# Performance work log

Measured on AMD Instinct MI355X. Metric: run time of the kernel, lower is better.

## Reference

```python
import math
import jax, jax.numpy as jnp
import numpy as np

B, T, C = 2, 2048, 1024
N_HEAD = 16
HEAD_DIM = C // N_HEAD


def setup_inputs() -> dict:
    key = jax.random.key(0)
    k1, k2, k3 = jax.random.split(key, 3)
    std = 0.02
    return {
        "x": jax.random.normal(k1, (B, T, C), dtype=jnp.float32),
        "W_qkv": jax.random.normal(k2, (3 * C, C), dtype=jnp.float32) * std,
        "b_qkv": jnp.zeros((3 * C,), dtype=jnp.float32),
        "W_proj": jax.random.normal(k3, (C, C), dtype=jnp.float32) * std,
        "b_proj": jnp.zeros((C,), dtype=jnp.float32),
    }


def reference(x, W_qkv, b_qkv, W_proj, b_proj):
    Bs, Ts, Cs = x.shape
    # qkv projection, split as [3][n_head][head_dim] along last dim (matches torch view order)
    qkv = (x @ W_qkv.T + b_qkv).reshape(Bs, Ts, 3, N_HEAD, HEAD_DIM)
    qkv = qkv.transpose(0, 3, 2, 1, 4)  # (B, H, 3, T, hd)
    q, k, v = qkv[:, :, 0], qkv[:, :, 1], qkv[:, :, 2]  # each (B, H, T, hd)
    scale = 1.0 / math.sqrt(HEAD_DIM)
    att = jnp.einsum('bhtd,bhsd->bhts', q, k) * scale  # (B, H, T, T)
    causal = jnp.tril(jnp.ones((Ts, Ts), dtype=bool))
    att = jnp.where(causal, att, -jnp.inf)
    att = jax.nn.softmax(att, axis=-1)
    y = jnp.einsum('bhts,bhsd->bhtd', att, v)  # (B, H, T, hd)
    y = y.transpose(0, 2, 1, 3).reshape(Bs, Ts, Cs)
    return y @ W_proj.T + b_proj
```

## Files before the change

kernel.cpp:

```cpp
#include <hip/hip_runtime.h>
#include <cstdint>

#define BDIM  2
#define TSEQ  2048
#define CDIM  1024
#define NHEAD 16
#define HDIM  64
#define C3    3072

typedef __attribute__((ext_vector_type(8))) short short8_t;
typedef __attribute__((ext_vector_type(4))) short short4_t;
typedef __attribute__((ext_vector_type(4))) float f32x4;

static __device__ __forceinline__ unsigned short f2bf(float f) {
  union { float f; unsigned u; } v; v.f = f;
  unsigned r = v.u + 0x7FFFu + ((v.u >> 16) & 1u);
  return (unsigned short)(r >> 16);
}
static __device__ __forceinline__ unsigned cvtpk_bf16(float lo, float hi) {
  unsigned r;
  asm("v_cvt_pk_bf16_f32 %0, %1, %2" : "=v"(r) : "v"(lo), "v"(hi));
  return r;
}
static __device__ __forceinline__ void g2lds16(const unsigned short* g,
                                               unsigned short* l) {
  __builtin_amdgcn_global_load_lds(
      (const __attribute__((address_space(1))) void*)g,
      (__attribute__((address_space(3))) void*)l, 16, 0, 0);
}

__device__ __forceinline__ int kk_idx(int row, int chunk) {
  return row * 64 + (((chunk ^ (row & 7)) & 7) << 3);
}
__device__ __forceinline__ int vv_idx(int d, int chunk) {
  return d * 64 + (((chunk ^ (d & 7) ^ ((d >> 3) & 7)) & 7) << 3);
}

__global__ __launch_bounds__(256) void f32_to_bf16_3(
    const float* __restrict__ x, const float* __restrict__ wq,
    const float* __restrict__ wp, unsigned short* __restrict__ outb,
    int n1, int n2, int n3)
{
  const int i = blockIdx.x * 256 + threadIdx.x;
  const float* src; unsigned short* dst; int j;
  if (i < n1)            { src = x;  dst = outb;                        j = i; }
  else if (i < n1 + n2)  { src = wq; dst = outb + (size_t)n1 * 4;       j = i - n1; }
  else if (i < n1+n2+n3) { src = wp; dst = outb + (size_t)(n1+n2) * 4;  j = i - n1 - n2; }
  else return;
  const float4 v = ((const float4*)src)[j];
  const unsigned lo = (unsigned)f2bf(v.x) | ((unsigned)f2bf(v.y) << 16);
  const unsigned hi = (unsigned)f2bf(v.z) | ((unsigned)f2bf(v.w) << 16);
  ((uint2*)dst)[j] = make_uint2(lo, hi);
}

template <int FJ, bool OUT_BF16>
__global__ __launch_bounds__(256, 2) void gemm_bt_mfma(
    const unsigned short* __restrict__ A, const unsigned short* __restrict__ B,
    const float* __restrict__ bias, void* __restrict__ Cv,
    int M, int N, int K)
{
  __shared__ unsigned short As[128 * 64];
  __shared__ unsigned short Bs[FJ * 32 * 64];

  const int tid  = threadIdx.x;
  const int lane = tid & 63;
  const int wv   = tid >> 6;
  const int wr   = wv >> 1, wc = wv & 1;
  const int l15  = lane & 15, g = lane >> 4;
  const int bn = blockIdx.x, bm = blockIdx.y;

  const int srow = tid >> 3;
  const int chg  = (tid & 7) ^ (srow & 7);
  const unsigned short* Ab = A + (size_t)(bm * 128 + srow) * K + chg * 8;
  const unsigned short* Bb = B + (size_t)(bn * (FJ * 32) + srow) * K + chg * 8;

  f32x4 acc[4][FJ];
#pragma unroll
  for (int i = 0; i < 4; ++i)
#pragma unroll
    for (int j = 0; j < FJ; ++j) acc[i][j] = (f32x4){0.f, 0.f, 0.f, 0.f};

  for (int k0 = 0; k0 < K; k0 += 64) {
    __syncthreads();
#pragma unroll
    for (int c = 0; c < 4; ++c)
      g2lds16(Ab + (size_t)(c * 32) * K + k0, &As[c * 2048 + wv * 512]);
#pragma unroll
    for (int c = 0; c < FJ; ++c)
      g2lds16(Bb + (size_t)(c * 32) * K + k0, &Bs[c * 2048 + wv * 512]);
    __syncthreads();

#pragma unroll
    for (int kk = 0; kk < 2; ++kk) {
      short8_t af[4], bf[FJ];
#pragma unroll
      for (int i = 0; i < 4; ++i)
        af[i] = *(const short8_t*)&As[kk_idx(wr * 64 + i * 16 + l15, kk * 4 + g)];
#pragma unroll
      for (int j = 0; j < FJ; ++j)
        bf[j] = *(const short8_t*)&Bs[kk_idx(wc * (FJ * 16) + j * 16 + l15, kk * 4 + g)];
#pragma unroll
      for (int i = 0; i < 4; ++i)
#pragma unroll
        for (int j = 0; j < FJ; ++j)
          acc[i][j] = __builtin_amdgcn_mfma_f32_16x16x32_bf16(af[i], bf[j], acc[i][j], 0, 0, 0);
    }
  }

#pragma unroll
  for (int j = 0; j < FJ; ++j) {
    const int col = bn * (FJ * 32) + wc * (FJ * 16) + j * 16 + l15;
    const float bj = bias[col];
#pragma unroll
    for (int i = 0; i < 4; ++i) {
#pragma unroll
      for (int r = 0; r < 4; ++r) {
        const int row = bm * 128 + wr * 64 + i * 16 + g * 4 + r;
        const float v = acc[i][j][r] + bj;
        if (OUT_BF16) ((unsigned short*)Cv)[(size_t)row * N + col] = f2bf(v);
        else          ((float*)Cv)[(size_t)row * N + col] = v;
      }
    }
  }
}

__global__ __launch_bounds__(512, 2) void attn_mfma(
    const unsigned short* __restrict__ qkv, unsigned short* __restrict__ yb)
{
  __shared__ unsigned short SM[21504];
  unsigned short* Ks = SM;
  unsigned short* Vt = SM + 8192;
  unsigned short* Ps = SM + 16384;

  const int tid  = threadIdx.x;
  const int lane = tid & 63;
  const int wv   = tid >> 6;
  const int qs   = wv & 3;
  const int kvh  = wv >> 2;
  const int l15  = lane & 15, g = lane >> 4;

  const int nfl = blockIdx.x;
  const int x   = (nfl >> 3) & 15;
  const int grp = (nfl & 7) | ((nfl >> 7) << 3);
  const int h = grp & 15, b = grp >> 4;

  const unsigned short* kbase = qkv + (size_t)(b * TSEQ) * C3 + CDIM + h * HDIM;
  const unsigned short* vbase = kbase + CDIM;
  unsigned short* Pw = &Ps[wv * 640];

  const float SC2 = 0.18033688011112042f;
  const float THR = 11.5415603f;

  const int skv = tid >> 3, sc = tid & 7;
  const int kwo = kk_idx(skv, sc);
  const int vs = tid >> 4, dh = (tid >> 3) & 1, va = tid & 7;
  int vwo[4];
#pragma unroll
  for (int j = 0; j < 4; ++j)
    vwo[j] = vv_idx(va * 8 + dh * 4 + j, vs >> 2) + ((2 * vs) & 7);

  int tg = 0;

  for (int ph = 0; ph < 2; ++ph) {
    const int qt   = ph ? (31 - x) : x;
    const int wq0  = qt * 64 + qs * 16;
    const int q_hi = wq0 + 15;
    const int qg   = wq0 + l15;
    const int ntiles = qt + 1;

    short8_t qf[2];
#pragma unroll
    for (int kk = 0; kk < 2; ++kk)
      qf[kk] = *(const short8_t*)(qkv +
          (size_t)(b * TSEQ + wq0 + l15) * C3 + h * HDIM + kk * 32 + g * 8);

    f32x4 O[4];
#pragma unroll
    for (int n = 0; n < 4; ++n) O[n] = (f32x4){0.f, 0.f, 0.f, 0.f};
    float Mr = 0.0f, Lr = 0.f;

    const unsigned short* kptr  = kbase + (size_t)skv * C3 + sc * 8;
    const unsigned short* vptr0 = vbase + (size_t)(2 * vs) * C3 + va * 8 + dh * 4;
    const unsigned short* vptr1 = vptr0 + C3;
    short8_t pk  = *(const short8_t*)(kptr);
    short4_t pv0 = *(const short4_t*)(vptr0);
    short4_t pv1 = *(const short4_t*)(vptr1);

    for (int t = 0; t < ntiles; ++t) {
      const int par = tg & 1;
      unsigned short* Kc = &Ks[par * 4096];
      unsigned short* Vc = &Vt[par * 4096];
      tg++;
      *(short8_t*)&Kc[kwo] = pk;
      {
        const unsigned short* e0 = (const unsigned short*)&pv0;
        const unsigned short* e1 = (const unsigned short*)&pv1;
#pragma unroll
        for (int j = 0; j < 4; ++j)
          *(unsigned*)&Vc[vwo[j]] = (unsigned)e0[j] | ((unsigned)e1[j] << 16);
      }
      __syncthreads();
      if (t + 1 < ntiles) {
        kptr  += (size_t)64 * C3;
        vptr0 += (size_t)64 * C3;
        vptr1 += (size_t)64 * C3;
        pk  = *(const short8_t*)(kptr);
        pv0 = *(const short4_t*)(vptr0);
        pv1 = *(const short4_t*)(vptr1);
      }
      const int kvw0 = t * 64 + kvh * 32;
      if (kvw0 > q_hi) continue;
      const int nl = (q_hi - kvw0) >> 4;
      const int nlim = (nl > 1) ? 1 : nl;

      f32x4 s[2];
#pragma unroll
      for (int n = 0; n < 2; ++n) s[n] = (f32x4){0.f, 0.f, 0.f, 0.f};
      __builtin_amdgcn_s_setprio(1);
#pragma unroll
      for (int n = 0; n < 2; ++n) {
        if (n <= nlim) {
#pragma unroll
          for (int kk = 0; kk < 2; ++kk) {
            const short8_t kf =
                *(const short8_t*)&Kc[kk_idx(kvh * 32 + n * 16 + l15, kk * 4 + g)];
            s[n] = __builtin_amdgcn_mfma_f32_16x16x32_bf16(kf, qf[kk], s[n], 0, 0, 0);
          }
        }
      }
      __builtin_amdgcn_s_setprio(0);

      float mt = -3.0e38f;
#pragma unroll
      for (int n = 0; n < 2; ++n) {
        if (n <= nlim) {
          const int kvb = kvw0 + n * 16 + g * 4;
          const bool needmask = (kvw0 + n * 16 + 15 > wq0);
#pragma unroll
          for (int r = 0; r < 4; ++r) {
            float v = s[n][r] * SC2;
            if (needmask && (kvb + r > qg)) v = -3.0e38f;
            s[n][r] = v;
            mt = fmaxf(mt, v);
          }
        }
      }

      float rs = 0.f;
#pragma unroll
      for (int n = 0; n < 2; ++n) {
        if (n <= nlim) {
#pragma unroll
          for (int r = 0; r < 4; ++r) {
            const float p = __builtin_amdgcn_exp2f(s[n][r] - Mr);
            s[n][r] = p;
            rs += p;
          }
        }
      }
#pragma unroll
      for (int n = 0; n < 2; ++n) {
        const unsigned u0 = cvtpk_bf16(s[n][0], s[n][1]);
        const unsigned u1 = cvtpk_bf16(s[n][2], s[n][3]);
        *(uint2*)&Pw[l15 * 40 + n * 16 + (g << 2)] = make_uint2(u0, u1);
      }
      mt = fmaxf(mt, __shfl_xor(mt, 16));
      mt = fmaxf(mt, __shfl_xor(mt, 32));
      if (__any(mt > Mr + THR)) {
        const float nm = fmaxf(Mr, mt);
        const float al = __builtin_amdgcn_exp2f(Mr - nm);
        Lr *= al;
        rs *= al;
        float alq[4];
#pragma unroll
        for (int r = 0; r < 4; ++r) alq[r] = __shfl(al, (g << 2) + r);
#pragma unroll
        for (int n = 0; n < 4; ++n)
#pragma unroll
          for (int r = 0; r < 4; ++r) O[n][r] *= alq[r];
        Mr = nm;
#pragma unroll
        for (int n = 0; n < 2; ++n) {
          if (n <= nlim) {
#pragma unroll
            for (int r = 0; r < 4; ++r) s[n][r] *= al;
          }
          const unsigned u0 = cvtpk_bf16(s[n][0], s[n][1]);
          const unsigned u1 = cvtpk_bf16(s[n][2], s[n][3]);
          *(uint2*)&Pw[l15 * 40 + n * 16 + (g << 2)] = make_uint2(u0, u1);
        }
      }

      const short8_t pf = *(const short8_t*)&Pw[l15 * 40 + g * 8];
      __builtin_amdgcn_s_setprio(1);
#pragma unroll
      for (int n = 0; n < 4; ++n) {
        const short8_t vf = *(const short8_t*)&Vc[vv_idx(n * 16 + l15, kvh * 4 + g)];
        O[n] = __builtin_amdgcn_mfma_f32_16x16x32_bf16(pf, vf, O[n], 0, 0, 0);
      }
      __builtin_amdgcn_s_setprio(0);

      rs += __shfl_xor(rs, 16);
      rs += __shfl_xor(rs, 32);
      Lr += rs;
    }

    __syncthreads();
    {
      float* Cb = (float*)SM;
      const int slot = (qs * 64 + lane) * 18;
      if (kvh == 1) {
#pragma unroll
        for (int n = 0; n < 4; ++n)
#pragma unroll
          for (int r = 0; r < 4; ++r) Cb[slot + n * 4 + r] = O[n][r];
        Cb[slot + 16] = Mr;
        Cb[slot + 17] = Lr;
      }
    }
    __syncthreads();
    if (kvh == 0) {
      const float* Cb = (const float*)SM;
      const int slot = (qs * 64 + lane) * 18;
      const float m2 = Cb[slot + 16], l2 = Cb[slot + 17];
      const float m  = fmaxf(Mr, m2);
      const float a1 = __builtin_amdgcn_exp2f(Mr - m);
      const float a2 = __builtin_amdgcn_exp2f(m2 - m);
      const float inv = 1.0f / (Lr * a1 + l2 * a2);
      const float fa = a1 * inv, fb = a2 * inv;
      float faq[4], fbq[4];
#pragma unroll
      for (int r = 0; r < 4; ++r) {
        faq[r] = __shfl(fa, (g << 2) + r);
        fbq[r] = __shfl(fb, (g << 2) + r);
      }
#pragma unroll
      for (int n = 0; n < 4; ++n)
#pragma unroll
        for (int r = 0; r < 4; ++r) {
          const float o2 = Cb[slot + n * 4 + r];
          const size_t row = (size_t)(b * TSEQ + wq0 + (g << 2) + r);
          yb[row * CDIM + h * HDIM + n * 16 + l15] =
              f2bf(O[n][r] * faq[r] + o2 * fbq[r]);
        }
    }
    __syncthreads();
  }
}

extern "C" void kernel_launch(void* const* d_in, const int* in_sizes, int n_in,
                              void* d_out, int out_size, void* d_ws, size_t ws_size,
                              hipStream_t stream)
{
  const float* x     = (const float*)d_in[0];
  const float* Wqkv  = (const float*)d_in[1];
  const float* bqkv  = (const float*)d_in[2];
  const float* Wproj = (const float*)d_in[3];
  const float* bproj = (const float*)d_in[4];
  float* out = (float*)d_out;

  const int M = BDIM * TSEQ;
  unsigned short* qkv = (unsigned short*)d_ws;
  unsigned short* yb  = qkv + (size_t)M * C3;
  unsigned short* xb  = yb  + (size_t)M * CDIM;
  unsigned short* wqb = xb  + (size_t)M * CDIM;
  unsigned short* wpb = wqb + (size_t)C3 * CDIM;

  const int n1 = M * CDIM / 4, n2 = C3 * CDIM / 4, n3 = CDIM * CDIM / 4;
  f32_to_bf16_3<<<(n1 + n2 + n3 + 255) / 256, 256, 0, stream>>>(
      x, Wqkv, Wproj, xb, n1, n2, n3);

  gemm_bt_mfma<4, true><<<dim3(C3 / 128, M / 128), 256, 0, stream>>>(
      xb, wqb, bqkv, (void*)qkv, M, C3, CDIM);

  attn_mfma<<<dim3(512, 1, 1), 512, 0, stream>>>(qkv, yb);

  gemm_bt_mfma<2, false><<<dim3(CDIM / 64, M / 128), 256, 0, stream>>>(
      yb, wpb, bproj, (void*)out, M, CDIM, CDIM);
}
```

Baseline: 107.5 us.

## Add unmasked fast path in attention, lighter barriers, and smaller proj GEMM tiles

Attention adds a fast path for fully unmasked KV tiles that skips per-element masking and fuses scale into the exp argument. It defers the cross-lane max reduction into the rare rescale branch and replaces __syncthreads with an lgkmcnt wait plus barrier. The combine buffer moves to a separate LDS region so the trailing barrier can go. The GEMM is templated on the M tile, and the output projection now uses 64x64 tiles with higher occupancy hints for more blocks.

```diff
diff --git a/kernel.cpp b/kernel.cpp
--- a/kernel.cpp
+++ b/kernel.cpp
@@ -27,6 +27,9 @@
   __builtin_amdgcn_global_load_lds(
       (const __attribute__((address_space(1))) void*)g,
       (__attribute__((address_space(3))) void*)l, 16, 0, 0);
+}
+static __device__ __forceinline__ void bar_lds() {
+  asm volatile("s_waitcnt lgkmcnt(0)\n\ts_barrier" ::: "memory");
 }
 
 __device__ __forceinline__ int kk_idx(int row, int chunk) {
@@ -53,13 +56,13 @@
   ((uint2*)dst)[j] = make_uint2(lo, hi);
 }
 
-template <int FJ, bool OUT_BF16>
-__global__ __launch_bounds__(256, 2) void gemm_bt_mfma(
+template <int FI, int FJ, bool OUT_BF16>
+__global__ __launch_bounds__(256, (FI == 4) ? 3 : 4) void gemm_bt_mfma(
     const unsigned short* __restrict__ A, const unsigned short* __restrict__ B,
     const float* __restrict__ bias, void* __restrict__ Cv,
     int M, int N, int K)
 {
-  __shared__ unsigned short As[128 * 64];
+  __shared__ unsigned short As[FI * 32 * 64];
   __shared__ unsigned short Bs[FJ * 32 * 64];
 
   const int tid  = threadIdx.x;
@@ -71,19 +74,19 @@
 
   const int srow = tid >> 3;
   const int chg  = (tid & 7) ^ (srow & 7);
-  const unsigned short* Ab = A + (size_t)(bm * 128 + srow) * K + chg * 8;
+  const unsigned short* Ab = A + (size_t)(bm * (FI * 32) + srow) * K + chg * 8;
   const unsigned short* Bb = B + (size_t)(bn * (FJ * 32) + srow) * K + chg * 8;
 
-  f32x4 acc[4][FJ];
-#pragma unroll
-  for (int i = 0; i < 4; ++i)
+  f32x4 acc[FI][FJ];
+#pragma unroll
+  for (int i = 0; i < FI; ++i)
 #pragma unroll
     for (int j = 0; j < FJ; ++j) acc[i][j] = (f32x4){0.f, 0.f, 0.f, 0.f};
 
   for (int k0 = 0; k0 < K; k0 += 64) {
     __syncthreads();
 #pragma unroll
-    for (int c = 0; c < 4; ++c)
+    for (int c = 0; c < FI; ++c)
       g2lds16(Ab + (size_t)(c * 32) * K + k0, &As[c * 2048 + wv * 512]);
 #pragma unroll
     for (int c = 0; c < FJ; ++c)
@@ -92,15 +95,15 @@
 
 #pragma unroll
     for (int kk = 0; kk < 2; ++kk) {
-      short8_t af[4], bf[FJ];
-#pragma unroll
-      for (int i = 0; i < 4; ++i)
-        af[i] = *(const short8_t*)&As[kk_idx(wr * 64 + i * 16 + l15, kk * 4 + g)];
+      short8_t af[FI], bf[FJ];
+#pragma unroll
+      for (int i = 0; i < FI; ++i)
+        af[i] = *(const short8_t*)&As[kk_idx(wr * (FI * 16) + i * 16 + l15, kk * 4 + g)];
 #pragma unroll
       for (int j = 0; j < FJ; ++j)
         bf[j] = *(const short8_t*)&Bs[kk_idx(wc * (FJ * 16) + j * 16 + l15, kk * 4 + g)];
 #pragma unroll
-      for (int i = 0; i < 4; ++i)
+      for (int i = 0; i < FI; ++i)
 #pragma unroll
         for (int j = 0; j < FJ; ++j)
           acc[i][j] = __builtin_amdgcn_mfma_f32_16x16x32_bf16(af[i], bf[j], acc[i][j], 0, 0, 0);
@@ -112,10 +115,10 @@
     const int col = bn * (FJ * 32) + wc * (FJ * 16) + j * 16 + l15;
     const float bj = bias[col];
 #pragma unroll
-    for (int i = 0; i < 4; ++i) {
+    for (int i = 0; i < FI; ++i) {
 #pragma unroll
       for (int r = 0; r < 4; ++r) {
-        const int row = bm * 128 + wr * 64 + i * 16 + g * 4 + r;
+        const int row = bm * (FI * 32) + wr * (FI * 16) + i * 16 + g * 4 + r;
         const float v = acc[i][j][r] + bj;
         if (OUT_BF16) ((unsigned short*)Cv)[(size_t)row * N + col] = f2bf(v);
         else          ((float*)Cv)[(size_t)row * N + col] = v;
@@ -127,7 +130,7 @@
 __global__ __launch_bounds__(512, 2) void attn_mfma(
     const unsigned short* __restrict__ qkv, unsigned short* __restrict__ yb)
 {
-  __shared__ unsigned short SM[21504];
+  __shared__ unsigned short SM[25600];
   unsigned short* Ks = SM;
   unsigned short* Vt = SM + 8192;
   unsigned short* Ps = SM + 16384;
@@ -147,6 +150,7 @@
   const unsigned short* kbase = qkv + (size_t)(b * TSEQ) * C3 + CDIM + h * HDIM;
   const unsigned short* vbase = kbase + CDIM;
   unsigned short* Pw = &Ps[wv * 640];
+  float* Cb = (float*)Ps;
 
   const float SC2 = 0.18033688011112042f;
   const float THR = 11.5415603f;
@@ -199,7 +203,7 @@
         for (int j = 0; j < 4; ++j)
           *(unsigned*)&Vc[vwo[j]] = (unsigned)e0[j] | ((unsigned)e1[j] << 16);
       }
-      __syncthreads();
+      bar_lds();
       if (t + 1 < ntiles) {
         kptr  += (size_t)64 * C3;
         vptr0 += (size_t)64 * C3;
@@ -210,8 +214,9 @@
       }
       const int kvw0 = t * 64 + kvh * 32;
       if (kvw0 > q_hi) continue;
+      const bool fullt = (kvw0 + 31 <= wq0);
       const int nl = (q_hi - kvw0) >> 4;
-      const int nlim = (nl > 1) ? 1 : nl;
+      const int nlim = fullt ? 1 : ((nl > 1) ? 1 : nl);
 
       f32x4 s[2];
 #pragma unroll
@@ -230,43 +235,58 @@
       }
       __builtin_amdgcn_s_setprio(0);
 
-      float mt = -3.0e38f;
-#pragma unroll
-      for (int n = 0; n < 2; ++n) {
-        if (n <= nlim) {
-          const int kvb = kvw0 + n * 16 + g * 4;
-          const bool needmask = (kvw0 + n * 16 + 15 > wq0);
+      float mt = -3.0e38f, rs = 0.f;
+      if (fullt) {
+#pragma unroll
+        for (int n = 0; n < 2; ++n)
+#pragma unroll
+          for (int r = 0; r < 4; ++r) mt = fmaxf(mt, s[n][r]);
+        mt *= SC2;
+#pragma unroll
+        for (int n = 0; n < 2; ++n)
 #pragma unroll
           for (int r = 0; r < 4; ++r) {
-            float v = s[n][r] * SC2;
-            if (needmask && (kvb + r > qg)) v = -3.0e38f;
-            s[n][r] = v;
-            mt = fmaxf(mt, v);
-          }
-        }
-      }
-
-      float rs = 0.f;
-#pragma unroll
-      for (int n = 0; n < 2; ++n) {
-        if (n <= nlim) {
-#pragma unroll
-          for (int r = 0; r < 4; ++r) {
-            const float p = __builtin_amdgcn_exp2f(s[n][r] - Mr);
+            const float p = __builtin_amdgcn_exp2f(fmaf(s[n][r], SC2, -Mr));
             s[n][r] = p;
             rs += p;
           }
-        }
-      }
+      } else {
+#pragma unroll
+        for (int n = 0; n < 2; ++n) {
+          if (n <= nlim) {
+            const int kvb = kvw0 + n * 16 + g * 4;
+            const bool needmask = (kvw0 + n * 16 + 15 > wq0);
+#pragma unroll
+            for (int r = 0; r < 4; ++r) {
+              float v = s[n][r] * SC2;
+              if (needmask && (kvb + r > qg)) v = -3.0e38f;
+              s[n][r] = v;
+              mt = fmaxf(mt, v);
+            }
+          }
+        }
+#pragma unroll
+        for (int n = 0; n < 2; ++n) {
+          if (n <= nlim) {
+#pragma unroll
+            for (int r = 0; r < 4; ++r) {
+              const float p = __builtin_amdgcn_exp2f(s[n][r] - Mr);
+              s[n][r] = p;
+              rs += p;
+            }
+          }
+        }
+      }
+
 #pragma unroll
       for (int n = 0; n < 2; ++n) {
         const unsigned u0 = cvtpk_bf16(s[n][0], s[n][1]);
         const unsigned u1 = cvtpk_bf16(s[n][2], s[n][3]);
         *(uint2*)&Pw[l15 * 40 + n * 16 + (g << 2)] = make_uint2(u0, u1);
       }
-      mt = fmaxf(mt, __shfl_xor(mt, 16));
-      mt = fmaxf(mt, __shfl_xor(mt, 32));
       if (__any(mt > Mr + THR)) {
+        mt = fmaxf(mt, __shfl_xor(mt, 16));
+        mt = fmaxf(mt, __shfl_xor(mt, 32));
         const float nm = fmaxf(Mr, mt);
         const float al = __builtin_amdgcn_exp2f(Mr - nm);
         Lr *= al;
@@ -281,10 +301,8 @@
         Mr = nm;
 #pragma unroll
         for (int n = 0; n < 2; ++n) {
-          if (n <= nlim) {
-#pragma unroll
-            for (int r = 0; r < 4; ++r) s[n][r] *= al;
-          }
+#pragma unroll
+          for (int r = 0; r < 4; ++r) s[n][r] *= al;
           const unsigned u0 = cvtpk_bf16(s[n][0], s[n][1]);
           const unsigned u1 = cvtpk_bf16(s[n][2], s[n][3]);
           *(uint2*)&Pw[l15 * 40 + n * 16 + (g << 2)] = make_uint2(u0, u1);
@@ -306,21 +324,17 @@
     }
 
     __syncthreads();
-    {
-      float* Cb = (float*)SM;
+    if (kvh == 1) {
       const int slot = (qs * 64 + lane) * 18;
-      if (kvh == 1) {
-#pragma unroll
-        for (int n = 0; n < 4; ++n)
-#pragma unroll
-          for (int r = 0; r < 4; ++r) Cb[slot + n * 4 + r] = O[n][r];
-        Cb[slot + 16] = Mr;
-        Cb[slot + 17] = Lr;
-      }
+#pragma unroll
+      for (int n = 0; n < 4; ++n)
+#pragma unroll
+        for (int r = 0; r < 4; ++r) Cb[slot + n * 4 + r] = O[n][r];
+      Cb[slot + 16] = Mr;
+      Cb[slot + 17] = Lr;
     }
     __syncthreads();
     if (kvh == 0) {
-      const float* Cb = (const float*)SM;
       const int slot = (qs * 64 + lane) * 18;
       const float m2 = Cb[slot + 16], l2 = Cb[slot + 17];
       const float m  = fmaxf(Mr, m2);
@@ -344,7 +358,6 @@
               f2bf(O[n][r] * faq[r] + o2 * fbq[r]);
         }
     }
-    __syncthreads();
   }
 }
 
@@ -370,11 +383,11 @@
   f32_to_bf16_3<<<(n1 + n2 + n3 + 255) / 256, 256, 0, stream>>>(
       x, Wqkv, Wproj, xb, n1, n2, n3);
 
-  gemm_bt_mfma<4, true><<<dim3(C3 / 128, M / 128), 256, 0, stream>>>(
+  gemm_bt_mfma<4, 4, true><<<dim3(C3 / 128, M / 128), 256, 0, stream>>>(
       xb, wqb, bqkv, (void*)qkv, M, C3, CDIM);
 
   attn_mfma<<<dim3(512, 1, 1), 512, 0, stream>>>(qkv, yb);
 
-  gemm_bt_mfma<2, false><<<dim3(CDIM / 64, M / 128), 256, 0, stream>>>(
+  gemm_bt_mfma<2, 2, false><<<dim3(CDIM / 64, M / 64), 256, 0, stream>>>(
       yb, wpb, bproj, (void*)out, M, CDIM, CDIM);
 }
```

Result: slower. 124.7 us (+16.1%).
